# Optimization experiments

Hardware: AMD Instinct MI355X
Metric: run time of the kernel (lower is better)

Reference implementation:

```python
import jax, jax.numpy as jnp
import numpy as np
from jax.scipy.linalg import expm

N_QUBITS = 13
N_LAYERS = 4  # ceil(log2(13))


def _apply_2axes(T, M, a0, a1):
    """Apply 4x4 matrix M to the pair of 2-dim axes (a0, a1) of tensor T."""
    nd = T.ndim
    T = jnp.moveaxis(T, (a0, a1), (nd - 2, nd - 1))
    s = T.shape
    T = (T.reshape(s[:-2] + (4,)) @ M.T).reshape(s)
    return jnp.moveaxis(T, (nd - 2, nd - 1), (a0, a1))


def _conv_pairs(n):
    pairs = [(2 * i, 2 * i + 1) for i in range(n // 2)]
    if n > 2:
        pairs += [(2 * i + 1, (2 * i + 2) % n) for i in range(n // 2)]
    return pairs


def _conv_state(psi, U, n):
    # psi: [B] + [2]*n pure state
    for q0, q1 in _conv_pairs(n):
        psi = _apply_2axes(psi, U, 1 + q0, 1 + q1)
    return psi


def _conv_dm(rho, U, n):
    # rho: [B] + [2]*n (rows) + [2]*n (cols); apply U on rows, U* on cols
    Uc = U.conj()
    for q0, q1 in _conv_pairs(n):
        rho = _apply_2axes(rho, U, 1 + q0, 1 + q1)
        rho = _apply_2axes(rho, Uc, 1 + n + q0, 1 + n + q1)
    return rho


def _pool_dm(rho, n):
    # measure-and-discard qubits 0..n//2-1 (with index shifting these are the
    # original even-indexed qubits); averaging over outcomes == partial trace.
    measured = [2 * i for i in range(n // 2)]
    cur = n
    for q in reversed(measured):  # descending so lower indices stay valid
        rho = jnp.trace(rho, axis1=1 + q, axis2=1 + cur + q)
        cur -= 1
    return rho, cur


def setup_inputs() -> dict:
    key = jax.random.key(0)
    k1, k2, k3, k4 = jax.random.split(key, 4)
    B, D = 2, 2 ** N_QUBITS
    return {
        "psi_real": jax.random.normal(k1, (B, D), dtype=jnp.float32),
        "psi_imag": jax.random.normal(k2, (B, D), dtype=jnp.float32),
        "H_real": jax.random.normal(k3, (N_LAYERS, 4, 4), dtype=jnp.float32),
        "H_imag": jax.random.normal(k4, (N_LAYERS, 4, 4), dtype=jnp.float32),
    }


def reference(psi_real, psi_imag, H_real, H_imag):
    B = psi_real.shape[0]
    n = N_QUBITS
    psi = (psi_real + 1j * psi_imag).astype(jnp.complex64)
    psi = psi / jnp.linalg.norm(psi, axis=1, keepdims=True)
    H = (H_real + 1j * H_imag).astype(jnp.complex64)
    # anti-hermitian generator -> unitary gate per layer
    Us = [expm(H[i] - H[i].conj().T) for i in range(N_LAYERS)]

    # layer 0: conv on pure state, then convert to density matrix, then pool
    psi = psi.reshape((B,) + (2,) * n)
    psi = _conv_state(psi, Us[0], n)
    flat = psi.reshape(B, -1)
    rho = (flat[:, :, None] * flat[:, None, :].conj()).reshape((B,) + (2,) * (2 * n))
    rho, n = _pool_dm(rho, n)

    for i in range(1, N_LAYERS):
        rho = _conv_dm(rho, Us[i], n)
        rho, n = _pool_dm(rho, n)

    # n == 1 here: measure qubit 0, return P(outcome 0)
    rho = rho.reshape(B, 2, 2)
    return rho[:, 0, 0].real
```

## Files before the change

kernel.cpp:

```cpp
#include <hip/hip_runtime.h>


#define NT 256
#define HDIM 4096

typedef float v2f __attribute__((ext_vector_type(2)));

__device__ __forceinline__ float2 cadds(float2 a, float2 b) {
    return make_float2(a.x + b.x, a.y + b.y);
}
__device__ __forceinline__ float2 cmacs(float2 acc, float2 a, float2 b) {
    acc.x = fmaf(a.x, b.x, fmaf(-a.y, b.y, acc.x));
    acc.y = fmaf(a.x, b.y, fmaf(a.y, b.x, acc.y));
    return acc;
}
__device__ __forceinline__ float2 shflc(float2 v, int src) {
    return make_float2(__shfl(v.x, src, 64), __shfl(v.y, src, 64));
}

__device__ __forceinline__ v2f cma(v2f acc, v2f u, v2f us, v2f a) {
#pragma clang fp contract(fast)
    v2f ax = __builtin_shufflevector(a, a, 0, 0);
    v2f ay = __builtin_shufflevector(a, a, 1, 1);
    acc = ax * u + acc;
    acc = ay * us + acc;
    return acc;
}

__device__ float2 expm_compute(float are, float aim) {
    const int lane = threadIdx.x & 63;
    const int e = lane & 15, r = e >> 2, c = e & 3;
    const int base = lane & 48;

    float v = fabsf(are) + fabsf(aim);
    v += __shfl_xor(v, 1, 64);
    v += __shfl_xor(v, 2, 64);
    v = fmaxf(v, __shfl_xor(v, 4, 64));
    v = fmaxf(v, __shfl_xor(v, 8, 64));
    v = fmaxf(v, __shfl_xor(v, 16, 64));
    v = fmaxf(v, __shfl_xor(v, 32, 64));

    int s = 0;
    while (v > 0.25f && s < 30) { v *= 0.5f; s++; }
    const float scale = ldexpf(1.0f, -s);

    float2 X = make_float2(are * scale, aim * scale);
    float2 E = X;
    if (r == c) E.x += 1.0f;
    float2 T = X;
    for (int k = 2; k <= 7; k++) {
        float2 acc = make_float2(0.f, 0.f);
        #pragma unroll
        for (int kk = 0; kk < 4; kk++) {
            float2 t = shflc(T, base + r * 4 + kk);
            float2 x = shflc(X, base + kk * 4 + c);
            acc = cmacs(acc, t, x);
        }
        const float inv = 1.0f / (float)k;
        T = make_float2(acc.x * inv, acc.y * inv);
        E = cadds(E, T);
    }
    for (int i = 0; i < s; i++) {
        float2 acc = make_float2(0.f, 0.f);
        #pragma unroll
        for (int kk = 0; kk < 4; kk++) {
            float2 a = shflc(E, base + r * 4 + kk);
            float2 bb = shflc(E, base + kk * 4 + c);
            acc = cmacs(acc, a, bb);
        }
        E = acc;
    }
    return E;
}

__device__ __forceinline__ void loadU(float2 E, int L, v2f* u, v2f* us) {
    #pragma unroll
    for (int k = 0; k < 16; k++) {
        float ur = __shfl(E.x, (L << 4) | k, 64);
        float ui = __shfl(E.y, (L << 4) | k, 64);
        u[k] = (v2f){ur, ui};
        us[k] = (v2f){-ui, ur};
    }
}

__device__ __forceinline__ int swz(int e) {
    return e ^ ((e >> 4) & 15) ^ ((e >> 8) & 15);
}

template<int MASK>
__device__ __forceinline__ int deposit(int t) {
    int r = 0;
    #pragma unroll
    for (int p = 0; p < 12; p++) {
        if (MASK & (1 << p)) { r |= (t & 1) << p; t >>= 1; }
    }
    return r;
}

template<int B3, int B2, int B1, int B0>
__device__ __forceinline__ int eaddr4(int base, int i) {
    return base | (((i >> 3) & 1) << B3) | (((i >> 2) & 1) << B2)
                | (((i >> 1) & 1) << B1) | ((i & 1) << B0);
}
template<int B2, int B1, int B0>
__device__ __forceinline__ int eaddr3(int base, int i) {
    return base | (((i >> 2) & 1) << B2) | (((i >> 1) & 1) << B1)
                | ((i & 1) << B0);
}

template<int B3, int B2, int B1, int B0, int MASK>
__device__ __forceinline__ void phase_read(v2f* v, const v2f* psi, int t) {
    const int base = deposit<MASK>(t);
    #pragma unroll
    for (int i = 0; i < 16; i++) v[i] = psi[swz(eaddr4<B3, B2, B1, B0>(base, i))];
}
template<int B3, int B2, int B1, int B0, int MASK>
__device__ __forceinline__ void phase_write(const v2f* v, v2f* psi, int t) {
    const int base = deposit<MASK>(t);
    #pragma unroll
    for (int i = 0; i < 16; i++) psi[swz(eaddr4<B3, B2, B1, B0>(base, i))] = v[i];
}

template<int B2, int B1, int B0, int MASK>
__device__ __forceinline__ void q_read(v2f* q, const v2f* psi, int t, int hb8) {
    const int base = deposit<MASK>(t) | hb8;
    #pragma unroll
    for (int i = 0; i < 8; i++) q[i] = psi[swz(eaddr3<B2, B1, B0>(base, i))];
}
template<int B2, int B1, int B0, int MASK>
__device__ __forceinline__ void q_write(const v2f* q, v2f* psi, int t, int hb8) {
    const int base = deposit<MASK>(t) | hb8;
    #pragma unroll
    for (int i = 0; i < 8; i++) psi[swz(eaddr3<B2, B1, B0>(base, i))] = q[i];
}

template<int KA, int KB>
__device__ __forceinline__ void apply_gate(v2f* v, const v2f* u, const v2f* us) {
    const int MA = 1 << KA, MB = 1 << KB;
    #pragma unroll
    for (int i = 0; i < 16; i++) {
        if (i & (MA | MB)) continue;
        v2f a0 = v[i], a1 = v[i | MB], a2 = v[i | MA], a3 = v[i | MA | MB];
        v2f z = {0.f, 0.f};
        v2f n0 = cma(cma(cma(cma(z, u[0], us[0], a0), u[1], us[1], a1),
                         u[2], us[2], a2), u[3], us[3], a3);
        v2f n1 = cma(cma(cma(cma(z, u[4], us[4], a0), u[5], us[5], a1),
                         u[6], us[6], a2), u[7], us[7], a3);
        v2f n2 = cma(cma(cma(cma(z, u[8], us[8], a0), u[9], us[9], a1),
                         u[10], us[10], a2), u[11], us[11], a3);
        v2f n3 = cma(cma(cma(cma(z, u[12], us[12], a0), u[13], us[13], a1),
                         u[14], us[14], a2), u[15], us[15], a3);
        v[i] = n0; v[i | MB] = n1; v[i | MA] = n2; v[i | MA | MB] = n3;
    }
}
template<int KA, int KB>
__device__ __forceinline__ void apply_gate3(v2f* v, const v2f* u, const v2f* us) {
    const int MA = 1 << KA, MB = 1 << KB;
    #pragma unroll
    for (int i = 0; i < 8; i++) {
        if (i & (MA | MB)) continue;
        v2f a0 = v[i], a1 = v[i | MB], a2 = v[i | MA], a3 = v[i | MA | MB];
        v2f z = {0.f, 0.f};
        v2f n0 = cma(cma(cma(cma(z, u[0], us[0], a0), u[1], us[1], a1),
                         u[2], us[2], a2), u[3], us[3], a3);
        v2f n1 = cma(cma(cma(cma(z, u[4], us[4], a0), u[5], us[5], a1),
                         u[6], us[6], a2), u[7], us[7], a3);
        v2f n2 = cma(cma(cma(cma(z, u[8], us[8], a0), u[9], us[9], a1),
                         u[10], us[10], a2), u[11], us[11], a3);
        v2f n3 = cma(cma(cma(cma(z, u[12], us[12], a0), u[13], us[13], a1),
                         u[14], us[14], a2), u[15], us[15], a3);
        v[i] = n0; v[i | MB] = n1; v[i | MA] = n2; v[i | MA | MB] = n3;
    }
}

__global__ __launch_bounds__(NT, 1) void qcnn_kernel(
    const float* __restrict__ pr, const float* __restrict__ pi,
    const float* __restrict__ Hr, const float* __restrict__ Hi,
    float* __restrict__ out) {
    __shared__ v2f psi[HDIM];
    __shared__ v2f red[NT / 64];
    const int t = threadIdx.x;
    const int blk = blockIdx.x;
    const int b = blk >> 2;
    const int h12 = (blk >> 1) & 1;
    const int hb8 = (blk & 1) << 8;
    const int lane = t & 63;
    const int m = lane >> 4, ee = lane & 15, r = ee >> 2, c = ee & 3;

    float hra = Hr[m * 16 + r * 4 + c], hrb = Hr[m * 16 + c * 4 + r];
    float hia = Hi[m * 16 + r * 4 + c], hib = Hi[m * 16 + c * 4 + r];

    const float* prb = pr + b * 2 * HDIM;
    const float* pib = pi + b * 2 * HDIM;
    v2f w[32];
    #pragma unroll
    for (int i = 0; i < 32; i++) {
        int g = (((i >> 4) & 1) << 12) | (((i >> 3) & 1) << 11)
              | (((i >> 2) & 1) << 10) | (((i >> 1) & 1) << 9)
              | ((i & 1) << 8) | t;
        w[i] = (v2f){prb[g], pib[g]};
    }

    float2 E = expm_compute(hra - hrb, hia + hib);

    float norm2 = 0.f;
    #pragma unroll
    for (int i = 0; i < 32; i++)
        norm2 = fmaf(w[i].x, w[i].x, fmaf(w[i].y, w[i].y, norm2));

    v2f u[16], us[16];
    loadU(E, 0, u, us);

    v2f v[16];
    #pragma unroll
    for (int i = 0; i < 8; i++) {
        v2f a0 = w[i], a1 = w[i | 8], a2 = w[i | 16], a3 = w[i | 24];
        v2f z = {0.f, 0.f};
        v2f lo, hi;
        if (h12 == 0) {
            lo = cma(cma(cma(cma(z, u[0], us[0], a0), u[1], us[1], a1),
                         u[2], us[2], a2), u[3], us[3], a3);
            hi = cma(cma(cma(cma(z, u[4], us[4], a0), u[5], us[5], a1),
                         u[6], us[6], a2), u[7], us[7], a3);
        } else {
            lo = cma(cma(cma(cma(z, u[8], us[8], a0), u[9], us[9], a1),
                         u[10], us[10], a2), u[11], us[11], a3);
            hi = cma(cma(cma(cma(z, u[12], us[12], a0), u[13], us[13], a1),
                         u[14], us[14], a2), u[15], us[15], a3);
        }
        v[i] = lo; v[i | 8] = hi;
    }
    apply_gate<2, 1>(v, u, us);
    apply_gate<3, 2>(v, u, us);
    phase_write<11, 10, 9, 8, 0x0FF>(v, psi, t);
    __syncthreads();

    phase_read<9, 8, 7, 6, 0xC3F>(v, psi, t);
    apply_gate<2, 1>(v, u, us);
    apply_gate<3, 2>(v, u, us);
    {
        const int base2 = deposit<0xC3F>(t);
        #pragma unroll
        for (int i = 0; i < 16; i++) {
            if ((((i >> 2) & 1) << 8) != hb8) continue;
            psi[swz(base2 | (((i >> 3) & 1) << 9) | (((i >> 2) & 1) << 8)
                          | (((i >> 1) & 1) << 7) | ((i & 1) << 6))] = v[i];
        }
    }
    __syncthreads();

    v2f q[8];

    q_read<2, 1, 0, 0xEF8>(q, psi, t, hb8);
    apply_gate3<2, 1>(q, u, us);
    apply_gate3<1, 0>(q, u, us);
    q_write<2, 1, 0, 0xEF8>(q, psi, t, hb8);
    __syncthreads();

    q_read<4, 3, 2, 0xEE3>(q, psi, t, hb8);
    apply_gate3<2, 1>(q, u, us);
    apply_gate3<1, 0>(q, u, us);
    q_write<4, 3, 2, 0xEE3>(q, psi, t, hb8);
    __syncthreads();

    q_read<6, 5, 4, 0xE8F>(q, psi, t, hb8);
    apply_gate3<2, 1>(q, u, us);
    apply_gate3<1, 0>(q, u, us);
    q_write<6, 5, 4, 0xE8F>(q, psi, t, hb8);
    __syncthreads();

    q_read<7, 6, 5, 0xE1F>(q, psi, t, hb8);
    apply_gate3<2, 1>(q, u, us);
    loadU(E, 1, u, us);
    apply_gate3<2, 0>(q, u, us);
    q_write<7, 6, 5, 0xE1F>(q, psi, t, hb8);
    __syncthreads();

    q_read<11, 9, 7, 0x47F>(q, psi, t, hb8);
    apply_gate3<2, 1>(q, u, us);
    apply_gate3<1, 0>(q, u, us);
    q_write<11, 9, 7, 0x47F>(q, psi, t, hb8);
    __syncthreads();

    q_read<5, 3, 1, 0xED5>(q, psi, t, hb8);
    apply_gate3<1, 0>(q, u, us);
    apply_gate3<2, 1>(q, u, us);
    q_write<5, 3, 1, 0xED5>(q, psi, t, hb8);
    __syncthreads();

    q_read<5, 1, 0, 0xEDC>(q, psi, t, hb8);
    apply_gate3<1, 0>(q, u, us);
    loadU(E, 2, u, us);
    apply_gate3<1, 0>(q, u, us);
    q_write<5, 1, 0, 0xEDC>(q, psi, t, hb8);
    __syncthreads();

    q_read<9, 5, 1, 0xCDD>(q, psi, t, hb8);
    apply_gate3<2, 1>(q, u, us);
    apply_gate3<1, 0>(q, u, us);
    q_write<9, 5, 1, 0xCDD>(q, psi, t, hb8);
    __syncthreads();

    q_read<9, 5, 0, 0xCDE>(q, psi, t, hb8);
    apply_gate3<0, 2>(q, u, us);
    loadU(E, 3, u, us);
    apply_gate3<1, 0>(q, u, us);

    float s0 = 0.f;
    #pragma unroll
    for (int i = 0; i < 8; i += 2)
        s0 = fmaf(q[i].x, q[i].x, fmaf(q[i].y, q[i].y, s0));

    #pragma unroll
    for (int off = 1; off < 64; off <<= 1) {
        s0 += __shfl_xor(s0, off, 64);
        norm2 += __shfl_xor(norm2, off, 64);
    }
    if (lane == 0) red[t >> 6] = (v2f){s0, norm2};
    __syncthreads();
    if (t == 0) {
        float S = 0.f, Nrm = 0.f;
        #pragma unroll
        for (int wv = 0; wv < NT / 64; wv++) { S += red[wv].x; Nrm += red[wv].y; }
        atomicAdd(&out[b], S / Nrm);
    }
}

extern "C" void kernel_launch(void* const* d_in, const int* in_sizes, int n_in,
                              void* d_out, int out_size, void* d_ws, size_t ws_size,
                              hipStream_t stream) {
    const float* pr = (const float*)d_in[0];
    const float* pi = (const float*)d_in[1];
    const float* Hr = (const float*)d_in[2];
    const float* Hi = (const float*)d_in[3];
    float* out = (float*)d_out;
    qcnn_kernel<<<dim3(out_size * 4), dim3(NT), 0, stream>>>(pr, pi, Hr, Hi, out);
}
```

Before: 68.44 us.

## Replace LDS round-trips with cross-lane shuffle gates after the second phase

```diff
diff --git a/kernel.cpp b/kernel.cpp
--- a/kernel.cpp
+++ b/kernel.cpp
@@ -16,6 +16,9 @@
 }
 __device__ __forceinline__ float2 shflc(float2 v, int src) {
     return make_float2(__shfl(v.x, src, 64), __shfl(v.y, src, 64));
+}
+__device__ __forceinline__ v2f shflx(v2f v, int mask) {
+    return (v2f){__shfl_xor(v.x, mask, 64), __shfl_xor(v.y, mask, 64)};
 }
 
 __device__ __forceinline__ v2f cma(v2f acc, v2f u, v2f us, v2f a) {
@@ -102,11 +105,6 @@
     return base | (((i >> 3) & 1) << B3) | (((i >> 2) & 1) << B2)
                 | (((i >> 1) & 1) << B1) | ((i & 1) << B0);
 }
-template<int B2, int B1, int B0>
-__device__ __forceinline__ int eaddr3(int base, int i) {
-    return base | (((i >> 2) & 1) << B2) | (((i >> 1) & 1) << B1)
-                | ((i & 1) << B0);
-}
 
 template<int B3, int B2, int B1, int B0, int MASK>
 __device__ __forceinline__ void phase_read(v2f* v, const v2f* psi, int t) {
@@ -119,19 +117,6 @@
     const int base = deposit<MASK>(t);
     #pragma unroll
     for (int i = 0; i < 16; i++) psi[swz(eaddr4<B3, B2, B1, B0>(base, i))] = v[i];
-}
-
-template<int B2, int B1, int B0, int MASK>
-__device__ __forceinline__ void q_read(v2f* q, const v2f* psi, int t, int hb8) {
-    const int base = deposit<MASK>(t) | hb8;
-    #pragma unroll
-    for (int i = 0; i < 8; i++) q[i] = psi[swz(eaddr3<B2, B1, B0>(base, i))];
-}
-template<int B2, int B1, int B0, int MASK>
-__device__ __forceinline__ void q_write(const v2f* q, v2f* psi, int t, int hb8) {
-    const int base = deposit<MASK>(t) | hb8;
-    #pragma unroll
-    for (int i = 0; i < 8; i++) psi[swz(eaddr3<B2, B1, B0>(base, i))] = q[i];
 }
 
 template<int KA, int KB>
@@ -154,7 +139,7 @@
     }
 }
 template<int KA, int KB>
-__device__ __forceinline__ void apply_gate3(v2f* v, const v2f* u, const v2f* us) {
+__device__ __forceinline__ void gate_rr(v2f* v, const v2f* u, const v2f* us) {
     const int MA = 1 << KA, MB = 1 << KB;
     #pragma unroll
     for (int i = 0; i < 8; i++) {
@@ -170,6 +155,67 @@
         v2f n3 = cma(cma(cma(cma(z, u[12], us[12], a0), u[13], us[13], a1),
                          u[14], us[14], a2), u[15], us[15], a3);
         v[i] = n0; v[i | MB] = n1; v[i | MA] = n2; v[i | MA | MB] = n3;
+    }
+}
+
+template<int LL, int MA, bool LANEMAJOR>
+__device__ __forceinline__ void gate_mx(v2f* q, const v2f* u) {
+    const int lane = threadIdx.x & 63;
+    const bool my = (lane >> LL) & 1;
+    v2f c[8], cs[8];
+    #pragma unroll
+    for (int s = 0; s < 2; s++) {
+        #pragma unroll
+        for (int j = 0; j < 4; j++) {
+            const int i0 = LANEMAJOR ? (s * 4 + j)
+                                     : (s * 8 + (((j & 1) << 1) | (j >> 1)));
+            const int ix = LANEMAJOR ? 10 : 5;
+            v2f cc = my ? u[i0 ^ ix] : u[i0];
+            c[s * 4 + j] = cc;
+            cs[s * 4 + j] = (v2f){-cc.y, cc.x};
+        }
+    }
+    v2f p[8];
+    #pragma unroll
+    for (int i = 0; i < 8; i++) p[i] = shflx(q[i], 1 << LL);
+    #pragma unroll
+    for (int i = 0; i < 8; i++) {
+        if (i & MA) continue;
+        v2f a0 = q[i], a1 = q[i | MA], a2 = p[i], a3 = p[i | MA];
+        v2f z = {0.f, 0.f};
+        v2f n0 = cma(cma(cma(cma(z, c[0], cs[0], a0), c[1], cs[1], a1),
+                         c[2], cs[2], a2), c[3], cs[3], a3);
+        v2f n1 = cma(cma(cma(cma(z, c[4], cs[4], a0), c[5], cs[5], a1),
+                         c[6], cs[6], a2), c[7], cs[7], a3);
+        q[i] = n0; q[i | MA] = n1;
+    }
+}
+
+template<int LA, int LB>
+__device__ __forceinline__ void gate_ll(v2f* q, const v2f* u) {
+    const int lane = threadIdx.x & 63;
+    const bool bA = (lane >> LA) & 1, bB = (lane >> LB) & 1;
+    v2f c[4], cs[4];
+    #pragma unroll
+    for (int j = 0; j < 4; j++) {
+        v2f t0 = bB ? u[4 + (1 ^ j)] : u[0 ^ j];
+        v2f t1 = bB ? u[12 + (3 ^ j)] : u[8 + (2 ^ j)];
+        v2f cc = bA ? t1 : t0;
+        c[j] = cc;
+        cs[j] = (v2f){-cc.y, cc.x};
+    }
+    v2f pB[8], pA[8], pAB[8];
+    #pragma unroll
+    for (int i = 0; i < 8; i++) pB[i] = shflx(q[i], 1 << LB);
+    #pragma unroll
+    for (int i = 0; i < 8; i++) pA[i] = shflx(q[i], 1 << LA);
+    #pragma unroll
+    for (int i = 0; i < 8; i++) pAB[i] = shflx(q[i], (1 << LA) | (1 << LB));
+    #pragma unroll
+    for (int i = 0; i < 8; i++) {
+        v2f z = {0.f, 0.f};
+        q[i] = cma(cma(cma(cma(z, c[0], cs[0], q[i]), c[1], cs[1], pB[i]),
+                       c[2], cs[2], pA[i]), c[3], cs[3], pAB[i]);
     }
 }
 
@@ -235,76 +281,52 @@
     phase_write<11, 10, 9, 8, 0x0FF>(v, psi, t);
     __syncthreads();
 
-    phase_read<9, 8, 7, 6, 0xC3F>(v, psi, t);
+    phase_read<11, 9, 8, 7, 0x47F>(v, psi, t);
+    apply_gate<1, 0>(v, u, us);
     apply_gate<2, 1>(v, u, us);
     apply_gate<3, 2>(v, u, us);
     {
-        const int base2 = deposit<0xC3F>(t);
+        const int base2 = deposit<0x47F>(t);
         #pragma unroll
         for (int i = 0; i < 16; i++) {
-            if ((((i >> 2) & 1) << 8) != hb8) continue;
-            psi[swz(base2 | (((i >> 3) & 1) << 9) | (((i >> 2) & 1) << 8)
-                          | (((i >> 1) & 1) << 7) | ((i & 1) << 6))] = v[i];
+            if ((((i >> 1) & 1) << 8) != hb8) continue;
+            psi[swz(base2 | (((i >> 3) & 1) << 11) | (((i >> 2) & 1) << 9)
+                          | (((i >> 1) & 1) << 8) | ((i & 1) << 7))] = v[i];
         }
     }
     __syncthreads();
 
+    const int ebase = (((t >> 7) & 1) << 11) | (((t >> 6) & 1) << 10)
+                    | (((lane >> 5) & 1) << 9) | hb8
+                    | (((lane >> 4) & 1) << 7) | (((lane >> 3) & 1) << 6)
+                    | (((lane >> 2) & 1) << 4) | (((lane >> 1) & 1) << 3)
+                    | ((lane & 1) << 2);
     v2f q[8];
-
-    q_read<2, 1, 0, 0xEF8>(q, psi, t, hb8);
-    apply_gate3<2, 1>(q, u, us);
-    apply_gate3<1, 0>(q, u, us);
-    q_write<2, 1, 0, 0xEF8>(q, psi, t, hb8);
-    __syncthreads();
-
-    q_read<4, 3, 2, 0xEE3>(q, psi, t, hb8);
-    apply_gate3<2, 1>(q, u, us);
-    apply_gate3<1, 0>(q, u, us);
-    q_write<4, 3, 2, 0xEE3>(q, psi, t, hb8);
-    __syncthreads();
-
-    q_read<6, 5, 4, 0xE8F>(q, psi, t, hb8);
-    apply_gate3<2, 1>(q, u, us);
-    apply_gate3<1, 0>(q, u, us);
-    q_write<6, 5, 4, 0xE8F>(q, psi, t, hb8);
-    __syncthreads();
-
-    q_read<7, 6, 5, 0xE1F>(q, psi, t, hb8);
-    apply_gate3<2, 1>(q, u, us);
+    #pragma unroll
+    for (int i = 0; i < 8; i++)
+        q[i] = psi[swz(ebase | (((i >> 2) & 1) << 5)
+                             | (((i >> 1) & 1) << 1) | (i & 1))];
+
+    gate_mx<3, 4, true>(q, u);
+    gate_ll<2, 1>(q, u);
+    gate_mx<0, 2, true>(q, u);
+    gate_ll<4, 3>(q, u);
+    gate_mx<2, 4, false>(q, u);
+    gate_ll<1, 0>(q, u);
+    gate_rr<1, 0>(q, u, us);
     loadU(E, 1, u, us);
-    apply_gate3<2, 0>(q, u, us);
-    q_write<7, 6, 5, 0xE1F>(q, psi, t, hb8);
-    __syncthreads();
-
-    q_read<11, 9, 7, 0x47F>(q, psi, t, hb8);
-    apply_gate3<2, 1>(q, u, us);
-    apply_gate3<1, 0>(q, u, us);
-    q_write<11, 9, 7, 0x47F>(q, psi, t, hb8);
-    __syncthreads();
-
-    q_read<5, 3, 1, 0xED5>(q, psi, t, hb8);
-    apply_gate3<1, 0>(q, u, us);
-    apply_gate3<2, 1>(q, u, us);
-    q_write<5, 3, 1, 0xED5>(q, psi, t, hb8);
-    __syncthreads();
-
-    q_read<5, 1, 0, 0xEDC>(q, psi, t, hb8);
-    apply_gate3<1, 0>(q, u, us);
+    gate_mx<4, 4, true>(q, u);
+    gate_mx<1, 2, true>(q, u);
+    gate_ll<5, 4>(q, u);
+    gate_mx<1, 4, false>(q, u);
+    gate_rr<1, 0>(q, u, us);
     loadU(E, 2, u, us);
-    apply_gate3<1, 0>(q, u, us);
-    q_write<5, 1, 0, 0xEDC>(q, psi, t, hb8);
-    __syncthreads();
-
-    q_read<9, 5, 1, 0xCDD>(q, psi, t, hb8);
-    apply_gate3<2, 1>(q, u, us);
-    apply_gate3<1, 0>(q, u, us);
-    q_write<9, 5, 1, 0xCDD>(q, psi, t, hb8);
-    __syncthreads();
-
-    q_read<9, 5, 0, 0xCDE>(q, psi, t, hb8);
-    apply_gate3<0, 2>(q, u, us);
+    gate_mx<5, 4, true>(q, u);
+    gate_rr<1, 0>(q, u, us);
+    gate_rr<2, 1>(q, u, us);
+    gate_mx<5, 1, false>(q, u);
     loadU(E, 3, u, us);
-    apply_gate3<1, 0>(q, u, us);
+    gate_rr<2, 0>(q, u, us);
 
     float s0 = 0.f;
     #pragma unroll
```

Result: slower. 119.6 us (+74.7%).
